# Kernel tuning notes

Hardware: AMD Instinct MI355X
Metric: run time of the kernel (lower is better)

Reference implementation:

```python
import jax, jax.numpy as jnp
import numpy as np

CHUNK = 1024  # query points processed per slab to avoid the full [N,M] matrix


def _nn_one(a, b):
    """Nearest-neighbor squared distance + index from each point in a [N,3] to set b [M,3]."""
    b_sq = jnp.sum(b * b, axis=-1)  # [M]

    def chunk_fn(ac):  # ac: [CHUNK, 3]
        # squared euclidean distance slab [CHUNK, M]
        d = jnp.sum(ac * ac, axis=-1)[:, None] + b_sq[None, :] - 2.0 * (ac @ b.T)
        return jnp.min(d, axis=-1), jnp.argmin(d, axis=-1).astype(jnp.int32)

    n = a.shape[0]
    a_chunks = a.reshape(n // CHUNK, CHUNK, 3)
    dmin, idx = jax.lax.map(chunk_fn, a_chunks)
    return dmin.reshape(n), idx.reshape(n)


def setup_inputs() -> dict:
    key = jax.random.key(0)
    k1, k2 = jax.random.split(key)
    B, N, M = 2, 16384, 16384
    xyz1 = jax.random.normal(k1, (B, N, 3), dtype=jnp.float32)
    xyz2 = jax.random.normal(k2, (B, M, 3), dtype=jnp.float32)
    return {"xyz1": xyz1, "xyz2": xyz2}


def reference(xyz1, xyz2):
    # ChamferDistanceFunction.forward with return_idx=True
    dist1, idx1 = jax.vmap(_nn_one)(xyz1, xyz2)  # [B,N], [B,N]
    dist2, idx2 = jax.vmap(_nn_one)(xyz2, xyz1)  # [B,M], [B,M]
    return dist1, dist2, idx1, idx2
```

## Files before the change

kernel.cpp:

```cpp
#include <hip/hip_runtime.h>

#define NPTS 16384
#define GRID 16
#define SGRID 8
#define NSB 512
#define NCELL 4096
#define CS_STRIDE (NCELL+1)
#define GLO -4.0f
#define GH 0.5f
#define GINVH 2.0f


__device__ __forceinline__ int clamp16(int v){ return v<0?0:(v>15?15:v); }
__device__ __forceinline__ int spr3(int v){
    return (v&1) | ((v&2)<<2) | ((v&4)<<4) | ((v&8)<<6);
}
__device__ __forceinline__ int mcode(int ix,int iy,int iz){
    return spr3(ix) | (spr3(iy)<<1) | (spr3(iz)<<2);
}

__global__ __launch_bounds__(256) void zero_hist(int* __restrict__ hist){
    hist[blockIdx.x*256 + threadIdx.x] = 0;
}

__global__ __launch_bounds__(256) void bin_kernel(
    const float* __restrict__ xyz1, const float* __restrict__ xyz2,
    int* __restrict__ hist)
{
    int t = blockIdx.x*256 + threadIdx.x;
    int s = t >> 14, i = t & (NPTS-1);
    const float* src = (s < 2 ? xyz1 : xyz2) + ((size_t)(s&1)*NPTS + i)*3;
    float x = src[0], y = src[1], z = src[2];
    int ix = clamp16((int)floorf((x-GLO)*GINVH));
    int iy = clamp16((int)floorf((y-GLO)*GINVH));
    int iz = clamp16((int)floorf((z-GLO)*GINVH));
    atomicAdd(&hist[s*NCELL + mcode(ix,iy,iz)], 1);
}

__global__ __launch_bounds__(1024) void scan_kernel(
    const int* __restrict__ hist, int* __restrict__ cellStart, int* __restrict__ cursor)
{
    int s = blockIdx.x, tid = threadIdx.x, lane = tid & 63, w = tid >> 6;
    const int* h = hist + s*NCELL;
    int v0 = h[tid*4+0], v1 = h[tid*4+1], v2 = h[tid*4+2], v3 = h[tid*4+3];
    int tsum = v0+v1+v2+v3;
    int x = tsum;
    #pragma unroll
    for (int d = 1; d < 64; d <<= 1) { int y = __shfl_up(x, d, 64); if (lane >= d) x += y; }
    __shared__ int wsum[16];
    if (lane == 63) wsum[w] = x;
    __syncthreads();
    if (tid == 0) { int acc = 0; for (int i2 = 0; i2 < 16; ++i2) { int tt = wsum[i2]; wsum[i2] = acc; acc += tt; } }
    __syncthreads();
    int excl = x - tsum + wsum[w];
    int* cs = cellStart + s*CS_STRIDE;
    int* cu = cursor   + s*NCELL;
    cs[tid*4+0] = excl; cu[tid*4+0] = excl; excl += v0;
    cs[tid*4+1] = excl; cu[tid*4+1] = excl; excl += v1;
    cs[tid*4+2] = excl; cu[tid*4+2] = excl; excl += v2;
    cs[tid*4+3] = excl; cu[tid*4+3] = excl; excl += v3;
    if (tid == 1023) cs[NCELL] = excl;
}

__global__ __launch_bounds__(256) void scatter_kernel(
    const float* __restrict__ xyz1, const float* __restrict__ xyz2,
    int* __restrict__ cursor, float4* __restrict__ spts, int* __restrict__ sidx)
{
    int t = blockIdx.x*256 + threadIdx.x;
    int s = t >> 14, i = t & (NPTS-1);
    const float* src = (s < 2 ? xyz1 : xyz2) + ((size_t)(s&1)*NPTS + i)*3;
    float x = src[0], y = src[1], z = src[2];
    float sq = __fadd_rn(__fadd_rn(__fmul_rn(x,x), __fmul_rn(y,y)), __fmul_rn(z,z));
    int ix = clamp16((int)floorf((x-GLO)*GINVH));
    int iy = clamp16((int)floorf((y-GLO)*GINVH));
    int iz = clamp16((int)floorf((z-GLO)*GINVH));
    int code = mcode(ix,iy,iz);
    int pos = atomicAdd(&cursor[s*NCELL + code], 1);
    spts[s*NPTS + pos] = make_float4(x, y, z, sq);
    sidx[s*NPTS + pos] = i;
}

__global__ __launch_bounds__(256) void nn_kernel(
    const float4* __restrict__ spts, const int* __restrict__ sidx,
    const int* __restrict__ cellStart, float* __restrict__ out)
{
    const int gt   = blockIdx.x*256 + threadIdx.x;
    const int lane = gt & 63;
    const int wv   = gt >> 6;
    const int set  = wv >> 11;
    const int dir  = set >> 1;
    const int b    = set & 1;
    const int qset = (dir == 0) ? b : 2 + b;
    const int cset = (dir == 0) ? 2 + b : b;
    const int wq    = wv & 2047;
    const int qbase = wq << 3;
    const int qsub  = lane >> 3;
    const int sub   = lane & 7;
    const int qpos  = qbase + qsub;

    __shared__ int sbS[NSB+1];
    {
        const int* csg = cellStart + cset*CS_STRIDE;
        for (int i = threadIdx.x; i <= NSB; i += 256) sbS[i] = csg[i << 3];
    }

    float4 q = spts[qset*NPTS + qpos];
    const int qorig = sidx[qset*NPTS + qpos];
    const float ax = q.x, ay = q.y, az = q.z, aw = q.w;

    int ix = clamp16((int)floorf((ax-GLO)*GINVH));
    int iy = clamp16((int)floorf((ay-GLO)*GINVH));
    int iz = clamp16((int)floorf((az-GLO)*GINVH));

    int bx0 = ix, bx1 = ix, by0 = iy, by1 = iy, bz0 = iz, bz1 = iz;
    #pragma unroll
    for (int m = 32; m; m >>= 1) {
        bx0 = min(bx0, __shfl_xor(bx0, m, 64)); bx1 = max(bx1, __shfl_xor(bx1, m, 64));
        by0 = min(by0, __shfl_xor(by0, m, 64)); by1 = max(by1, __shfl_xor(by1, m, 64));
        bz0 = min(bz0, __shfl_xor(bz0, m, 64)); bz1 = max(bz1, __shfl_xor(bz1, m, 64));
    }
    const int sx0 = __builtin_amdgcn_readfirstlane(bx0 >> 1);
    const int sx1 = __builtin_amdgcn_readfirstlane(bx1 >> 1);
    const int sy0 = __builtin_amdgcn_readfirstlane(by0 >> 1);
    const int sy1 = __builtin_amdgcn_readfirstlane(by1 >> 1);
    const int sz0 = __builtin_amdgcn_readfirstlane(bz0 >> 1);
    const int sz1 = __builtin_amdgcn_readfirstlane(bz1 >> 1);

    const float4* cp = spts + cset*NPTS;
    const int*    ci = sidx + cset*NPTS;

    __syncthreads();

    float bd = __builtin_inff(); int bi = 0;

    #define EVAL(c4, cix)                                                        \
    {                                                                            \
        float tt = fmaf(az, (c4).z, fmaf(ay, (c4).y, __fmul_rn(ax, (c4).x)));    \
        float dd = fmaf(-2.0f, tt, __fadd_rn(aw, (c4).w));                       \
        bool bet = (dd < bd) || (dd == bd && (cix) < bi);                        \
        bd = bet ? dd : bd; bi = bet ? (cix) : bi;                               \
    }

    #define SCAN_RANGE(j0, j1)                                                   \
    {                                                                            \
        int j = (j0) + sub;                                                      \
        for (; j + 24 < (j1); j += 32) {                                         \
            float4 c0 = cp[j];    int i0 = ci[j];                                \
            float4 c1 = cp[j+8];  int i1 = ci[j+8];                              \
            float4 c2 = cp[j+16]; int i2 = ci[j+16];                             \
            float4 c3 = cp[j+24]; int i3 = ci[j+24];                             \
            EVAL(c0, i0); EVAL(c1, i1); EVAL(c2, i2); EVAL(c3, i3);              \
        }                                                                        \
        for (; j < (j1); j += 8) {                                               \
            float4 c4 = cp[j]; int cix = ci[j];                                  \
            EVAL(c4, cix);                                                       \
        }                                                                        \
    }

    for (int s = 0; s <= 8; ++s) {
        int zlo = max(0, sz0 - s), zhi = min(SGRID-1, sz1 + s);
        int ylo = max(0, sy0 - s), yhi = min(SGRID-1, sy1 + s);
        int xlo = max(0, sx0 - s), xhi = min(SGRID-1, sx1 + s);
        for (int scz = zlo; scz <= zhi; ++scz) {
            int cdz = max(0, max(sz0 - scz, scz - sz1));
            float lo = (scz == 0)       ? -1e30f : (GLO + (float)(scz*2    )*GH);
            float hi = (scz == SGRID-1) ?  1e30f : (GLO + (float)(scz*2 + 2)*GH);
            float dzz = fmaxf(0.0f, fmaxf(lo - az, az - hi));
            float dz2 = __fmul_rn(dzz, dzz);
            for (int scy = ylo; scy <= yhi; ++scy) {
                int cdy = max(cdz, max(0, max(sy0 - scy, scy - sy1)));
                if (cdy > s) continue;
                lo = (scy == 0)       ? -1e30f : (GLO + (float)(scy*2    )*GH);
                hi = (scy == SGRID-1) ?  1e30f : (GLO + (float)(scy*2 + 2)*GH);
                float dyy = fmaxf(0.0f, fmaxf(lo - ay, ay - hi));
                float dyz2 = fmaf(dyy, dyy, dz2);
                int sbyz = (spr3(scy)<<1) | (spr3(scz)<<2);
                for (int scx = xlo; scx <= xhi; ++scx) {
                    int cd = max(cdy, max(0, max(sx0 - scx, scx - sx1)));
                    if (cd != s) continue;
                    lo = (scx == 0)       ? -1e30f : (GLO + (float)(scx*2    )*GH);
                    hi = (scx == SGRID-1) ?  1e30f : (GLO + (float)(scx*2 + 2)*GH);
                    float dxx = fmaxf(0.0f, fmaxf(lo - ax, ax - hi));
                    float lb = fmaf(dxx, dxx, dyz2);
                    if (__ballot(fmaf(0.995f, lb, -3e-4f) <= bd) == 0ULL) continue;
                    int sb = spr3(scx) | sbyz;
                    int j0 = __builtin_amdgcn_readfirstlane(sbS[sb]);
                    int j1 = __builtin_amdgcn_readfirstlane(sbS[sb+1]);
                    SCAN_RANGE(j0, j1);
                }
            }
        }
        float wmax = bd;
        #pragma unroll
        for (int m = 32; m; m >>= 1) wmax = fmaxf(wmax, __shfl_xor(wmax, m, 64));
        float rs = (float)s;
        if (fmaf(0.995f, rs*rs, -3e-4f) > wmax) break;
        if (xlo == 0 && ylo == 0 && zlo == 0 &&
            xhi == SGRID-1 && yhi == SGRID-1 && zhi == SGRID-1) break;
    }

    #undef SCAN_RANGE
    #undef EVAL

    #pragma unroll
    for (int m = 1; m < 8; m <<= 1) {
        float od = __shfl_xor(bd, m, 64);
        int   oi = __shfl_xor(bi, m, 64);
        bool bet = (od < bd) || (od == bd && oi < bi);
        bd = bet ? od : bd; bi = bet ? oi : bi;
    }

    if (sub == 0) {
        int off  = dir ? 32768 : 0;
        int slot = b*NPTS + qorig;
        out[off + slot]         = bd;
        out[65536 + off + slot] = (float)bi;
    }
}

__global__ __launch_bounds__(256) void nn_full(
    const float* __restrict__ xyz1, const float* __restrict__ xyz2,
    float* __restrict__ out)
{
    int qid = blockIdx.x*256 + threadIdx.x;
    int dir = qid >> 15;
    int q15 = qid & 32767;
    const float* qsrc = dir ? xyz2 : xyz1;
    float ax = qsrc[q15*3+0], ay = qsrc[q15*3+1], az = qsrc[q15*3+2];
    float asq = __fadd_rn(__fadd_rn(__fmul_rn(ax,ax), __fmul_rn(ay,ay)), __fmul_rn(az,az));
    const float* cp = (dir ? xyz1 : xyz2) + (size_t)(q15 & NPTS)*3;
    float bd = 3.402823466e+38f; int bi = 0;
    for (int j = 0; j < NPTS; ++j) {
        float bx = cp[3*j+0], by = cp[3*j+1], bz = cp[3*j+2];
        float bsq = __fadd_rn(__fadd_rn(__fmul_rn(bx,bx), __fmul_rn(by,by)), __fmul_rn(bz,bz));
        float tt = fmaf(az, bz, fmaf(ay, by, __fmul_rn(ax, bx)));
        float d = fmaf(-2.0f, tt, __fadd_rn(asq, bsq));
        if (d < bd) { bd = d; bi = j; }
    }
    int off = dir ? 32768 : 0;
    out[off + q15]         = bd;
    out[65536 + off + q15] = (float)bi;
}

extern "C" void kernel_launch(void* const* d_in, const int* in_sizes, int n_in,
                              void* d_out, int out_size, void* d_ws, size_t ws_size,
                              hipStream_t stream) {
    const float* xyz1 = (const float*)d_in[0];
    const float* xyz2 = (const float*)d_in[1];
    float* out = (float*)d_out;

    const size_t off_spts = 0;
    const size_t off_sidx = 1048576;
    const size_t off_cs   = 1310720;
    const size_t off_hist = 1376272;
    const size_t off_cur  = 1441808;
    const size_t need     = 1507344;

    if (d_ws != nullptr && ws_size >= need) {
        float4* spts = (float4*)((char*)d_ws + off_spts);
        int* sidx    = (int*)((char*)d_ws + off_sidx);
        int* cstart  = (int*)((char*)d_ws + off_cs);
        int* hist    = (int*)((char*)d_ws + off_hist);
        int* cursor  = (int*)((char*)d_ws + off_cur);
        zero_hist   <<<64,  256, 0, stream>>>(hist);
        bin_kernel  <<<256, 256, 0, stream>>>(xyz1, xyz2, hist);
        scan_kernel <<<4,  1024, 0, stream>>>(hist, cstart, cursor);
        scatter_kernel<<<256,256,0, stream>>>(xyz1, xyz2, cursor, spts, sidx);
        nn_kernel   <<<2048, 256, 0, stream>>>(spts, sidx, cstart, out);
    } else {
        nn_full<<<65536/256, 256, 0, stream>>>(xyz1, xyz2, out);
    }
}
```

Before: 197.9 us.

## Seed NN search with sorted neighbors and cull fine cells inside supercells

Before the supercell ring search, each wavefront scans a window of 160 candidates around its own position in the Morton-sorted array. This seeds a tight best-distance bound early. Inside each visited supercell, the 8 fine cells are now tested separately with per-cell lower bounds, and cells that cannot improve any lane are skipped. The shared-memory cellStart cache and its __syncthreads are removed in favour of direct global reads of 9 offsets, which trades LDS setup for more scalar loads and more per-cell branch overhead.

```diff
diff --git a/kernel.cpp b/kernel.cpp
--- a/kernel.cpp
+++ b/kernel.cpp
@@ -3,7 +3,6 @@
 #define NPTS 16384
 #define GRID 16
 #define SGRID 8
-#define NSB 512
 #define NCELL 4096
 #define CS_STRIDE (NCELL+1)
 #define GLO -4.0f
@@ -92,17 +91,10 @@
     const int b    = set & 1;
     const int qset = (dir == 0) ? b : 2 + b;
     const int cset = (dir == 0) ? 2 + b : b;
-    const int wq    = wv & 2047;
-    const int qbase = wq << 3;
+    const int qbase = (wv & 2047) << 3;
     const int qsub  = lane >> 3;
     const int sub   = lane & 7;
     const int qpos  = qbase + qsub;
-
-    __shared__ int sbS[NSB+1];
-    {
-        const int* csg = cellStart + cset*CS_STRIDE;
-        for (int i = threadIdx.x; i <= NSB; i += 256) sbS[i] = csg[i << 3];
-    }
 
     float4 q = spts[qset*NPTS + qpos];
     const int qorig = sidx[qset*NPTS + qpos];
@@ -128,8 +120,7 @@
 
     const float4* cp = spts + cset*NPTS;
     const int*    ci = sidx + cset*NPTS;
-
-    __syncthreads();
+    const int*    cs = cellStart + cset*CS_STRIDE;
 
     float bd = __builtin_inff(); int bi = 0;
 
@@ -157,6 +148,14 @@
         }                                                                        \
     }
 
+    {
+        int s0 = qbase + 4 - 80; if (s0 < 0) s0 = 0;
+        int e0 = s0 + 160;       if (e0 > NPTS) { e0 = NPTS; s0 = e0 - 160; }
+        s0 = __builtin_amdgcn_readfirstlane(s0);
+        e0 = __builtin_amdgcn_readfirstlane(e0);
+        SCAN_RANGE(s0, e0);
+    }
+
     for (int s = 0; s <= 8; ++s) {
         int zlo = max(0, sz0 - s), zhi = min(SGRID-1, sz1 + s);
         int ylo = max(0, sy0 - s), yhi = min(SGRID-1, sy1 + s);
@@ -167,6 +166,12 @@
             float hi = (scz == SGRID-1) ?  1e30f : (GLO + (float)(scz*2 + 2)*GH);
             float dzz = fmaxf(0.0f, fmaxf(lo - az, az - hi));
             float dz2 = __fmul_rn(dzz, dzz);
+            float zl0 = (scz == 0)       ? -1e30f : (GLO + (float)(scz*2    )*GH);
+            float zh0 =                              GLO + (float)(scz*2 + 1)*GH;
+            float zl1 =                              GLO + (float)(scz*2 + 1)*GH;
+            float zh1 = (scz == SGRID-1) ?  1e30f : (GLO + (float)(scz*2 + 2)*GH);
+            float dzc0 = fmaxf(0.0f, fmaxf(zl0 - az, az - zh0)); float dz0q = dzc0*dzc0;
+            float dzc1 = fmaxf(0.0f, fmaxf(zl1 - az, az - zh1)); float dz1q = dzc1*dzc1;
             for (int scy = ylo; scy <= yhi; ++scy) {
                 int cdy = max(cdz, max(0, max(sy0 - scy, scy - sy1)));
                 if (cdy > s) continue;
@@ -174,6 +179,11 @@
                 hi = (scy == SGRID-1) ?  1e30f : (GLO + (float)(scy*2 + 2)*GH);
                 float dyy = fmaxf(0.0f, fmaxf(lo - ay, ay - hi));
                 float dyz2 = fmaf(dyy, dyy, dz2);
+                float yl0 = (scy == 0)       ? -1e30f : (GLO + (float)(scy*2    )*GH);
+                float yh0 =                              GLO + (float)(scy*2 + 1)*GH;
+                float yh1 = (scy == SGRID-1) ?  1e30f : (GLO + (float)(scy*2 + 2)*GH);
+                float dyc0 = fmaxf(0.0f, fmaxf(yl0 - ay, ay - yh0)); float dy0q = dyc0*dyc0;
+                float dyc1 = fmaxf(0.0f, fmaxf(yh0 - ay, ay - yh1)); float dy1q = dyc1*dyc1;
                 int sbyz = (spr3(scy)<<1) | (spr3(scz)<<2);
                 for (int scx = xlo; scx <= xhi; ++scx) {
                     int cd = max(cdy, max(0, max(sx0 - scx, scx - sx1)));
@@ -184,9 +194,24 @@
                     float lb = fmaf(dxx, dxx, dyz2);
                     if (__ballot(fmaf(0.995f, lb, -3e-4f) <= bd) == 0ULL) continue;
                     int sb = spr3(scx) | sbyz;
-                    int j0 = __builtin_amdgcn_readfirstlane(sbS[sb]);
-                    int j1 = __builtin_amdgcn_readfirstlane(sbS[sb+1]);
-                    SCAN_RANGE(j0, j1);
+                    int base = sb << 3;
+                    int o[9];
+                    #pragma unroll
+                    for (int k = 0; k < 9; ++k)
+                        o[k] = __builtin_amdgcn_readfirstlane(cs[base + k]);
+                    float xl0 = (scx == 0)       ? -1e30f : (GLO + (float)(scx*2    )*GH);
+                    float xh0 =                              GLO + (float)(scx*2 + 1)*GH;
+                    float xh1 = (scx == SGRID-1) ?  1e30f : (GLO + (float)(scx*2 + 2)*GH);
+                    float dxc0 = fmaxf(0.0f, fmaxf(xl0 - ax, ax - xh0)); float dx0q = dxc0*dxc0;
+                    float dxc1 = fmaxf(0.0f, fmaxf(xh0 - ax, ax - xh1)); float dx1q = dxc1*dxc1;
+                    #pragma unroll
+                    for (int c = 0; c < 8; ++c) {
+                        float clb = ((c&1) ? dx1q : dx0q)
+                                  + ((c&2) ? dy1q : dy0q)
+                                  + ((c&4) ? dz1q : dz0q);
+                        if (__ballot(fmaf(0.995f, clb, -3e-4f) <= bd) == 0ULL) continue;
+                        SCAN_RANGE(o[c], o[c+1]);
+                    }
                 }
             }
         }
```

After: 247.1 us. 24.8% more time.
